# Kernel optimization log

Measured on AMD Instinct MI355X. Metric: run time of the kernel, lower is better.

Reference implementation:

```python
import jax, jax.numpy as jnp
import numpy as np


def setup_inputs() -> dict:
    key = jax.random.key(0)
    k1, k2, k3 = jax.random.split(key, 3)
    B, L, A = 131072, 40, 21  # batch of CDR3 sequences, seq len, amino-acid alphabet
    x = jax.random.uniform(k1, (B, L, A), dtype=jnp.float32)
    v_germline_aa_onehot = jax.random.uniform(k2, (L, A), dtype=jnp.float32)
    j_germline_aa_onehot = jax.random.uniform(k3, (L, A), dtype=jnp.float32)
    return {
        "x": x,
        "v_germline_aa_onehot": v_germline_aa_onehot,
        "j_germline_aa_onehot": j_germline_aa_onehot,
    }


def reference(x, v_germline_aa_onehot, j_germline_aa_onehot):
    # Per-position match score with the V germline: sum over amino-acid axis.
    v_match = jnp.einsum("bla,la->bl", x, v_germline_aa_onehot)  # [B, L]
    # Cumulative product along sequence positions (contiguous-match score),
    # then sum over positions -> expected length of contiguous V match.
    v_score = jnp.sum(jnp.cumprod(v_match, axis=1), axis=1)      # [B]
    # Total J-germline overlap: sum over all positions and amino acids.
    j_score = jnp.einsum("bla,la->b", x, j_germline_aa_onehot)   # [B]
    return jnp.stack([v_score, j_score], axis=-1)                # [B, 2]
```

## Files before the change

kernel.cpp:

```cpp
#include <hip/hip_runtime.h>

#define LPOS 40
#define AA   21
#define ROWF (LPOS*AA)
#define CPOS 2
#define CF   (CPOS*AA)
#define CF2  (CF/2)
#define NCH  (LPOS/CPOS)
#define ROWS 256
#define NTHR 256

__global__ __launch_bounds__(NTHR) void cm_kernel(
    const float* __restrict__ x,
    const float* __restrict__ v,
    const float* __restrict__ j,
    float* __restrict__ out)
{
    __shared__ float2 sx[ROWS * CF2];

    const int tid = threadIdx.x;
    const long long row0 = (long long)blockIdx.x * ROWS;
    const float2* __restrict__ x2 = (const float2*)x;

    float run = 1.0f, vsum = 0.0f, jsum = 0.0f;

    for (int c = 0; c < NCH; ++c) {
        __syncthreads();
        #pragma unroll
        for (int i = 0; i < (ROWS * CF2) / NTHR; ++i) {
            const int g = tid + i * NTHR;
            const int r = g / CF2;
            const int e = g - r * CF2;
            sx[g] = x2[(row0 + r) * (ROWF / 2) + c * CF2 + e];
        }
        __syncthreads();
        const float* __restrict__ xs = (const float*)&sx[tid * CF2];
        #pragma unroll
        for (int p = 0; p < CPOS; ++p) {
            const int l = c * CPOS + p;
            float m = 0.0f;
            #pragma unroll
            for (int a = 0; a < AA; ++a) {
                const float xv = xs[p * AA + a];
                m    = fmaf(xv, v[l * AA + a], m);
                jsum = fmaf(xv, j[l * AA + a], jsum);
            }
            run  *= m;
            vsum += run;
        }
    }

    const long long orow = row0 + tid;
    ((float2*)out)[orow] = make_float2(vsum, jsum);
}

extern "C" void kernel_launch(void* const* d_in, const int* in_sizes, int n_in,
                              void* d_out, int out_size, void* d_ws, size_t ws_size,
                              hipStream_t stream) {
    const float* x = (const float*)d_in[0];
    const float* v = (const float*)d_in[1];
    const float* j = (const float*)d_in[2];
    float* out     = (float*)d_out;

    const int B    = in_sizes[0] / ROWF;
    const int grid = B / ROWS;

    cm_kernel<<<grid, NTHR, 0, stream>>>(x, v, j, out);
}
```

Before: 98.00 us.

## Double-buffer per-position chunks with register prefetch and precomputed offsets

Each block now stages one sequence position (21 floats per row) at a time into a two-slot shared buffer. The next position's global loads go into registers while the current position is computed, so load latency overlaps compute and only one barrier is needed per step. Gather offsets are precomputed once per thread to avoid per-iteration division. The cost is 40 barriers instead of 20, scalar rather than float2 global loads with small per-row segments, and more registers for the prefetch array.

```diff
diff --git a/kernel.cpp b/kernel.cpp
--- a/kernel.cpp
+++ b/kernel.cpp
@@ -3,67 +3,88 @@
 #define LPOS 40
 #define AA   21
 #define ROWF (LPOS*AA)
-#define CPOS 2
-#define CF   (CPOS*AA)
-#define CF2  (CF/2)
-#define NCH  (LPOS/CPOS)
 #define ROWS 256
 #define NTHR 256
+#define CHF  (ROWS*AA)
+#define NIT  (CHF/NTHR)
 
 __global__ __launch_bounds__(NTHR) void cm_kernel(
     const float* __restrict__ x,
-    const float* __restrict__ v,
-    const float* __restrict__ j,
+    const float* __restrict__ vg,
+    const float* __restrict__ jg,
     float* __restrict__ out)
 {
-    __shared__ float2 sx[ROWS * CF2];
+    __shared__ float buf[2][CHF];
 
     const int tid = threadIdx.x;
     const long long row0 = (long long)blockIdx.x * ROWS;
-    const float2* __restrict__ x2 = (const float2*)x;
+    const float* __restrict__ xb = x + row0 * ROWF;
+
+    int goff[NIT];
+    {
+        int r = tid / AA;
+        int e = tid - r * AA;
+        int off = r * ROWF + e;
+        #pragma unroll
+        for (int i = 0; i < NIT; ++i) {
+            goff[i] = off;
+            e += 4; off += 12 * ROWF + 4;
+            if (e >= AA) { e -= AA; off += ROWF - AA; }
+        }
+    }
+
+    float rg[NIT];
+
+    #pragma unroll
+    for (int i = 0; i < NIT; ++i) rg[i] = xb[goff[i]];
+    #pragma unroll
+    for (int i = 0; i < NIT; ++i) buf[0][tid + i * NTHR] = rg[i];
+    #pragma unroll
+    for (int i = 0; i < NIT; ++i) rg[i] = xb[AA + goff[i]];
+    __syncthreads();
 
     float run = 1.0f, vsum = 0.0f, jsum = 0.0f;
 
-    for (int c = 0; c < NCH; ++c) {
-        __syncthreads();
-        #pragma unroll
-        for (int i = 0; i < (ROWS * CF2) / NTHR; ++i) {
-            const int g = tid + i * NTHR;
-            const int r = g / CF2;
-            const int e = g - r * CF2;
-            sx[g] = x2[(row0 + r) * (ROWF / 2) + c * CF2 + e];
+    #pragma unroll 2
+    for (int c = 0; c < LPOS; ++c) {
+        if (c < LPOS - 1) {
+            float* __restrict__ bo = buf[(c + 1) & 1];
+            #pragma unroll
+            for (int i = 0; i < NIT; ++i) bo[tid + i * NTHR] = rg[i];
         }
-        __syncthreads();
-        const float* __restrict__ xs = (const float*)&sx[tid * CF2];
-        #pragma unroll
-        for (int p = 0; p < CPOS; ++p) {
-            const int l = c * CPOS + p;
+        if (c < LPOS - 2) {
+            const float* __restrict__ xc = xb + (c + 2) * AA;
+            #pragma unroll
+            for (int i = 0; i < NIT; ++i) rg[i] = xc[goff[i]];
+        }
+        {
+            const float* __restrict__ xs = &buf[c & 1][tid * AA];
             float m = 0.0f;
             #pragma unroll
             for (int a = 0; a < AA; ++a) {
-                const float xv = xs[p * AA + a];
-                m    = fmaf(xv, v[l * AA + a], m);
-                jsum = fmaf(xv, j[l * AA + a], jsum);
+                const float xv = xs[a];
+                m    = fmaf(xv, vg[c * AA + a], m);
+                jsum = fmaf(xv, jg[c * AA + a], jsum);
             }
             run  *= m;
             vsum += run;
         }
+        __syncthreads();
     }
 
-    const long long orow = row0 + tid;
-    ((float2*)out)[orow] = make_float2(vsum, jsum);
+    ((float2*)out)[row0 + tid] = make_float2(vsum, jsum);
 }
 
 extern "C" void kernel_launch(void* const* d_in, const int* in_sizes, int n_in,
                               void* d_out, int out_size, void* d_ws, size_t ws_size,
                               hipStream_t stream) {
-    const float* x = (const float*)d_in[0];
-    const float* v = (const float*)d_in[1];
-    const float* j = (const float*)d_in[2];
-    float* out     = (float*)d_out;
+    const float* x  = (const float*)d_in[0];
+    const float* vg = (const float*)d_in[1];
+    const float* jg = (const float*)d_in[2];
+    float* out      = (float*)d_out;
 
     const int B    = in_sizes[0] / ROWF;
     const int grid = B / ROWS;
 
-    cm_kernel<<<grid, NTHR, 0, stream>>>(x, v, j, out);
+    cm_kernel<<<grid, NTHR, 0, stream>>>(x, vg, jg, out);
 }
```

New measurement: 109.9 us. +12.1%, slower.

## Use single-wavefront blocks with register double-buffered prefetch and no barriers

Applied to the files above, without the earlier changes.

Blocks shrink to one 64-lane wavefront, so the __syncthreads barriers are dropped and shared memory is accessed in wave-synchronous order, with compiler memory fences in place of barriers. Each chunk of x is loaded into registers two chunks ahead, using two alternating register buffers, then written to shared memory for transposed per-row reads. This is meant to hide global load latency behind compute and remove barrier stalls. The cost is higher register pressure and reliance on lockstep wavefront execution without real synchronisation, which is fragile.

```diff
diff --git a/kernel.cpp b/kernel.cpp
--- a/kernel.cpp
+++ b/kernel.cpp
@@ -7,63 +7,99 @@
 #define CF   (CPOS*AA)
 #define CF2  (CF/2)
 #define NCH  (LPOS/CPOS)
-#define ROWS 256
-#define NTHR 256
+#define NTHR 64
+
+#define FENCE() asm volatile("" ::: "memory")
 
 __global__ __launch_bounds__(NTHR) void cm_kernel(
     const float* __restrict__ x,
-    const float* __restrict__ v,
-    const float* __restrict__ j,
+    const float* __restrict__ vg,
+    const float* __restrict__ jg,
     float* __restrict__ out)
 {
-    __shared__ float2 sx[ROWS * CF2];
+    __shared__ float2 sbuf[NTHR * CF2];
 
-    const int tid = threadIdx.x;
-    const long long row0 = (long long)blockIdx.x * ROWS;
-    const float2* __restrict__ x2 = (const float2*)x;
+    const int lane = threadIdx.x;
+    const long long row0 = (long long)blockIdx.x * NTHR;
+    const float2* xw2 = (const float2*)x + row0 * (ROWF / 2);
+
+    int goff[CF2];
+    {
+        int r = lane / AA;
+        int e = lane - r * AA;
+        int off = r * (ROWF / 2) + e;
+        #pragma unroll
+        for (int i = 0; i < CF2; ++i) {
+            goff[i] = off;
+            e += 1; off += 3 * (ROWF / 2) + 1;
+            if (e >= AA) { e -= AA; off += (ROWF / 2) - AA; }
+        }
+    }
+
+    float2 rgA[CF2], rgB[CF2];
+
+    #pragma unroll
+    for (int i = 0; i < CF2; ++i) rgA[i] = xw2[goff[i]];
+    #pragma unroll
+    for (int i = 0; i < CF2; ++i) rgB[i] = xw2[goff[i] + CF2];
+    FENCE();
+    #pragma unroll
+    for (int i = 0; i < CF2; ++i) sbuf[lane + i * 64] = rgA[i];
+    FENCE();
+    #pragma unroll
+    for (int i = 0; i < CF2; ++i) rgA[i] = xw2[goff[i] + 2 * CF2];
+    FENCE();
 
     float run = 1.0f, vsum = 0.0f, jsum = 0.0f;
 
-    for (int c = 0; c < NCH; ++c) {
-        __syncthreads();
-        #pragma unroll
-        for (int i = 0; i < (ROWS * CF2) / NTHR; ++i) {
-            const int g = tid + i * NTHR;
-            const int r = g / CF2;
-            const int e = g - r * CF2;
-            sx[g] = x2[(row0 + r) * (ROWF / 2) + c * CF2 + e];
-        }
-        __syncthreads();
-        const float* __restrict__ xs = (const float*)&sx[tid * CF2];
-        #pragma unroll
-        for (int p = 0; p < CPOS; ++p) {
-            const int l = c * CPOS + p;
-            float m = 0.0f;
-            #pragma unroll
-            for (int a = 0; a < AA; ++a) {
-                const float xv = xs[p * AA + a];
-                m    = fmaf(xv, v[l * AA + a], m);
-                jsum = fmaf(xv, j[l * AA + a], jsum);
-            }
-            run  *= m;
-            vsum += run;
-        }
+    #define BODY(c, RGW)                                                   \
+      {                                                                    \
+        const float* xs = (const float*)&sbuf[lane * CF2];                 \
+        float m0 = 0.f, m1 = 0.f, jm = 0.f;                                \
+        _Pragma("unroll")                                                  \
+        for (int a = 0; a < AA; ++a) {                                     \
+          const float x0 = xs[a];                                          \
+          const float x1 = xs[AA + a];                                     \
+          m0 = fmaf(x0, vg[(c) * CF + a], m0);         \
+          m1 = fmaf(x1, vg[(c) * CF + AA + a], m1);                        \
+          jm = fmaf(x0, jg[(c) * CF + a], jm);                             \
+          jm = fmaf(x1, jg[(c) * CF + AA + a], jm);                        \
+        }                                                                  \
+        run *= m0; vsum += run;                                            \
+        run *= m1; vsum += run;                                            \
+        jsum += jm;                                                        \
+        FENCE();                                                           \
+        if ((c) + 1 < NCH) {                                               \
+          _Pragma("unroll")                                                \
+          for (int i = 0; i < CF2; ++i) sbuf[lane + i * 64] = RGW[i];      \
+          FENCE();                                                         \
+          if ((c) + 3 < NCH) {                                             \
+            _Pragma("unroll")                                              \
+            for (int i = 0; i < CF2; ++i)                                  \
+              RGW[i] = xw2[goff[i] + ((c) + 3) * CF2];                     \
+            FENCE();                                                       \
+          }                                                                \
+        }                                                                  \
+      }
+
+    for (int c = 0; c < NCH; c += 2) {
+        BODY(c,     rgB)
+        BODY(c + 1, rgA)
     }
 
-    const long long orow = row0 + tid;
-    ((float2*)out)[orow] = make_float2(vsum, jsum);
+    ((float2*)out)[row0 + lane] = make_float2(vsum, jsum);
 }
 
 extern "C" void kernel_launch(void* const* d_in, const int* in_sizes, int n_in,
                               void* d_out, int out_size, void* d_ws, size_t ws_size,
                               hipStream_t stream) {
-    const float* x = (const float*)d_in[0];
-    const float* v = (const float*)d_in[1];
-    const float* j = (const float*)d_in[2];
-    float* out     = (float*)d_out;
+    const float* x  = (const float*)d_in[0];
+    const float* vg = (const float*)d_in[1];
+    const float* jg = (const float*)d_in[2];
+    float* out      = (float*)d_out;
 
     const int B    = in_sizes[0] / ROWF;
-    const int grid = B / ROWS;
+    const int grid = B / NTHR;
 
-    cm_kernel<<<grid, NTHR, 0, stream>>>(x, v, j, out);
+    cm_kernel<<<grid, NTHR, 0, stream>>>(x, vg, jg, out);
 }
```

After: 86.66 us. 11.6% less time.

## Replace LDS-staged chunk loads with per-thread float4 register double-buffering

Applied to the files above, without the earlier changes.

Drops the shared-memory staging of two-position chunks, which needed two barriers per chunk. Each thread now reads its own row straight from global memory as float4 vectors, four positions at a time, into two register buffers so the next load overlaps the current compute. The cost is uncoalesced, strided access: adjacent threads read addresses 3360 bytes apart, so each wave load instruction touches many cache lines. The double buffers also raise register pressure and may lower occupancy.

```diff
diff --git a/kernel.cpp b/kernel.cpp
--- a/kernel.cpp
+++ b/kernel.cpp
@@ -3,67 +3,74 @@
 #define LPOS 40
 #define AA   21
 #define ROWF (LPOS*AA)
-#define CPOS 2
-#define CF   (CPOS*AA)
-#define CF2  (CF/2)
-#define NCH  (LPOS/CPOS)
-#define ROWS 256
+#define BODYP 4
+#define BODYF (BODYP*AA)
+#define BODY4 (BODYF/4)
+#define NBODY (LPOS/BODYP)
 #define NTHR 256
+
+#define EL(buf, i) (((i) & 3) == 0 ? buf[(i) >> 2].x : \
+                    ((i) & 3) == 1 ? buf[(i) >> 2].y : \
+                    ((i) & 3) == 2 ? buf[(i) >> 2].z : buf[(i) >> 2].w)
 
 __global__ __launch_bounds__(NTHR) void cm_kernel(
     const float* __restrict__ x,
-    const float* __restrict__ v,
-    const float* __restrict__ j,
+    const float* __restrict__ vg,
+    const float* __restrict__ jg,
     float* __restrict__ out)
 {
-    __shared__ float2 sx[ROWS * CF2];
+    const long long row = (long long)blockIdx.x * NTHR + threadIdx.x;
+    const float4* xr = (const float4*)(x + row * ROWF);
 
-    const int tid = threadIdx.x;
-    const long long row0 = (long long)blockIdx.x * ROWS;
-    const float2* __restrict__ x2 = (const float2*)x;
+    float4 bufA[BODY4], bufB[BODY4];
+
+    #define COMPUTE(k, BUF)                                                \
+      {                                                                    \
+        _Pragma("unroll")                                                  \
+        for (int p = 0; p < BODYP; ++p) {                                  \
+          float m = 0.f, jm = 0.f;                                         \
+          _Pragma("unroll")                                                \
+          for (int a = 0; a < AA; ++a) {                                   \
+            const int i = p * AA + a;                                      \
+            const float xv = EL(BUF, i);                                   \
+            m  = fmaf(xv, vg[(k) * BODYF + i], m);                         \
+            jm = fmaf(xv, jg[(k) * BODYF + i], jm);                        \
+          }                                                                \
+          run *= m; vsum += run; jsum += jm;                               \
+        }                                                                  \
+      }
+
+    #define LOAD(k, BUF)                                                   \
+      {                                                                    \
+        _Pragma("unroll")                                                  \
+        for (int i = 0; i < BODY4; ++i) BUF[i] = xr[(k) * BODY4 + i];      \
+      }
 
     float run = 1.0f, vsum = 0.0f, jsum = 0.0f;
 
-    for (int c = 0; c < NCH; ++c) {
-        __syncthreads();
-        #pragma unroll
-        for (int i = 0; i < (ROWS * CF2) / NTHR; ++i) {
-            const int g = tid + i * NTHR;
-            const int r = g / CF2;
-            const int e = g - r * CF2;
-            sx[g] = x2[(row0 + r) * (ROWF / 2) + c * CF2 + e];
-        }
-        __syncthreads();
-        const float* __restrict__ xs = (const float*)&sx[tid * CF2];
-        #pragma unroll
-        for (int p = 0; p < CPOS; ++p) {
-            const int l = c * CPOS + p;
-            float m = 0.0f;
-            #pragma unroll
-            for (int a = 0; a < AA; ++a) {
-                const float xv = xs[p * AA + a];
-                m    = fmaf(xv, v[l * AA + a], m);
-                jsum = fmaf(xv, j[l * AA + a], jsum);
-            }
-            run  *= m;
-            vsum += run;
-        }
+    LOAD(0, bufA)
+    #pragma unroll
+    for (int kk = 0; kk < NBODY / 2; ++kk) {
+        const int k = 2 * kk;
+        LOAD(k + 1, bufB)
+        COMPUTE(k, bufA)
+        if (k + 2 < NBODY) LOAD(k + 2, bufA)
+        COMPUTE(k + 1, bufB)
     }
 
-    const long long orow = row0 + tid;
-    ((float2*)out)[orow] = make_float2(vsum, jsum);
+    ((float2*)out)[row] = make_float2(vsum, jsum);
 }
 
 extern "C" void kernel_launch(void* const* d_in, const int* in_sizes, int n_in,
                               void* d_out, int out_size, void* d_ws, size_t ws_size,
                               hipStream_t stream) {
-    const float* x = (const float*)d_in[0];
-    const float* v = (const float*)d_in[1];
-    const float* j = (const float*)d_in[2];
-    float* out     = (float*)d_out;
+    const float* x  = (const float*)d_in[0];
+    const float* vg = (const float*)d_in[1];
+    const float* jg = (const float*)d_in[2];
+    float* out      = (float*)d_out;
 
     const int B    = in_sizes[0] / ROWF;
-    const int grid = B / ROWS;
+    const int grid = B / NTHR;
 
-    cm_kernel<<<grid, NTHR, 0, stream>>>(x, v, j, out);
+    cm_kernel<<<grid, NTHR, 0, stream>>>(x, vg, jg, out);
 }
```

New measurement: 176.6 us. +80.2%, slower.
